# Performance work log

Measured on AMD Instinct MI355X. Metric: run time of the kernel, lower is better.

Reference implementation:

```python
import jax, jax.numpy as jnp
from jax import lax
import numpy as np

FACTOR = 2
KERNEL = 3  # conv kernel size (odd)
DN = ('NCDHW', 'OIDHW', 'NCDHW')


def _setup_fir_kernel():
    # resample_kernel = (1,3,3,1); separable outer product, normalized, * factor**3 gain
    k1 = jnp.asarray([1.0, 3.0, 3.0, 1.0], dtype=jnp.float32)
    k = jnp.einsum('i,j,k->ijk', k1, k1, k1)
    k = k / jnp.sum(k)
    return k * (FACTOR ** 3)  # [4,4,4]


def _upfirdn3d_1x1(x, k, pad0, pad1):
    # upfirdn3d with up=down=1: pad then depthwise-correlate with flipped FIR kernel
    # (torch code runs F.conv3d with torch.flip(kernel)).
    n, c = x.shape[0], x.shape[1]
    xp = jnp.pad(x, ((0, 0), (0, 0), (pad0, pad1), (pad0, pad1), (pad0, pad1)))
    kf = jnp.flip(k).astype(x.dtype)  # flip all 3 spatial axes
    w = jnp.broadcast_to(kf[None, None], (c, 1) + k.shape)  # depthwise [C,1,4,4,4]
    return lax.conv_general_dilated(xp, w, (1, 1, 1), 'VALID',
                                    dimension_numbers=DN,
                                    feature_group_count=c)


def _upsample_conv_3d(x, weight):
    # Equivalent of upsample_conv_3d(x, w, k=(1,3,3,1), factor=2):
    # torch flips the weight and feeds conv_transpose3d(stride=2); the flip and
    # the implicit transpose-flip cancel, so it equals an lhs-dilated correlation
    # with the ORIGINAL weight, padded by (k-1) on each side (output_padding=0).
    k = _setup_fir_kernel()
    p = k.shape[0] - FACTOR - (KERNEL - 1)  # = 0
    pad_lo, pad_hi = (p + 1) // 2 + FACTOR - 1, p // 2 + 1  # = (1, 1)
    y = lax.conv_general_dilated(
        x, weight.astype(x.dtype), (1, 1, 1),
        padding=[(KERNEL - 1, KERNEL - 1)] * 3,
        lhs_dilation=(FACTOR, FACTOR, FACTOR),
        dimension_numbers=DN)  # [N, outC, 33, 33, 33]
    return _upfirdn3d_1x1(y, k, pad_lo, pad_hi)  # [N, outC, 32, 32, 32]


def setup_inputs() -> dict:
    key = jax.random.key(0)
    k1, k2, k3 = jax.random.split(key, 3)
    x = jax.random.normal(k1, (8, 256, 16, 16, 16), dtype=jnp.float32)
    weight = jax.random.normal(k2, (128, 256, 3, 3, 3), dtype=jnp.float32) * 0.05
    bias = jax.random.normal(k3, (128,), dtype=jnp.float32) * 0.05
    return {"x": x, "weight": weight, "bias": bias}


def reference(x, weight, bias):
    y = _upsample_conv_3d(x, weight)
    return y + bias.reshape(1, -1, 1, 1, 1)
```

## Files before the change

kernel.cpp:

```cpp
#include <hip/hip_runtime.h>
#include <string.h>

typedef __attribute__((ext_vector_type(4))) float f32x4;
typedef __attribute__((ext_vector_type(8))) _Float16 f16x8;
typedef unsigned short u16;
typedef unsigned int   u32;

#define NBATCH 8
#define ICN 256
#define OCN 128
#define VOLP 36432
#define WRE 884736
#define XTE 8388608
#define ZBF 4096
#define S1POOL 33792

__host__ __device__ constexpr int cls_yoff2(int c){
  return (c==0)?0:(c==1)?5168:(c==2)?9792:(c==3)?14416:
         (c==4)?18768:(c==5)?23632:(c==6)?27984:32336;
}
__host__ __device__ constexpr int cls_nxyp(int c){
  return ((c&3)==0)?304:((c&3)==3)?256:272;
}

__device__ __forceinline__ u16 f2h(float v){
  _Float16 h = (_Float16)v;
  u16 u; memcpy(&u, &h, 2);
  return u;
}

#define GLOAD16(gp, lp)                                                        \
  __builtin_amdgcn_global_load_lds(                                            \
      (const __attribute__((address_space(1))) void*)(gp),                     \
      (__attribute__((address_space(3))) void*)(lp), 16, 0, 0)

__global__ __launch_bounds__(256) void prep_w(const float* __restrict__ w,
                                              u16* __restrict__ wh,
                                              float* __restrict__ zb){
  if (blockIdx.x < 16) zb[blockIdx.x*256 + threadIdx.x] = 0.f;
  int idx = blockIdx.x*256 + threadIdx.x;
  int e = idx&7, ln=(idx>>3)&63, og=(idx>>9)&7, icc=(idx>>12)&7, tt=idx>>15;
  int oc = og*16 + (ln&15);
  int ic = icc*32 + ((ln>>4)&3)*8 + e;
  const int toffs[8] = {0,8,12,16,18,22,24,26};
  const int tcnt[8]  = {8,4,4,2,4,2,2,1};
  int c=0, t=0;
  #pragma unroll
  for (int cc=0; cc<8; ++cc)
    if (tt>=toffs[cc] && tt<toffs[cc]+tcnt[cc]){ c=cc; t=tt-toffs[cc]; }
  int ez=c>>2, ey=(c>>1)&1, ex=c&1;
  int ty=2-ey, tx=2-ex;
  int ax=t%tx, ay=(t/tx)%ty, az=t/(tx*ty);
  int qz = ez?1:(az?2:0), qy = ey?1:(ay?2:0), qx = ex?1:(ax?2:0);
  wh[idx] = f2h(w[((size_t)oc*ICN + ic)*27 + (qz*3+qy)*3+qx]);
}

__global__ __launch_bounds__(256) void prep_x(const float* __restrict__ x,
                                              u16* __restrict__ xh){
  u32 o = blockIdx.x*256 + threadIdx.x;
  int il = o & 31, p = (o>>5)&4095, icc = (o>>17)&7, n = o>>20;
  xh[o] = f2h(x[(size_t)(n*256 + icc*32 + il)*4096 + p]);
}

#define S1_ISSUE(BUFBYTE, ICCV, AZV)                                           \
  {                                                                            \
    _Pragma("unroll")                                                          \
    for (int j_=0; j_<3; ++j_){                                                \
      const int r_ = j_*64 + ln;                                               \
      if (r_ < 170){                                                           \
        const int s_ = wv*170 + r_;                                            \
        const int icg_ = s_&3, pos_ = s_>>2;                                   \
        const int xi_ = pos_%17, yi_ = pos_/17;                                \
        const int zc_ = EZ ? mz : (mz-1+(AZV));                                \
        const int yc_ = my0 + yi_ + (EY-1);                                    \
        const int xc_ = xi_ + (EX-1);                                          \
        const bool inb_ = (u32)zc_<16u && (u32)yc_<16u && (u32)xc_<16u;        \
        const size_t g_ = nbase + (size_t)(ICCV)*131072                        \
                        + (size_t)((zc_*256+yc_*16+xc_)*32 + icg_*8);          \
        const u16* gh_ = inb_ ? (xh+g_) : zb16;                                \
        char* lh_ = pool + (BUFBYTE) + s_*16;                                  \
        GLOAD16(gh_, lh_);                                                     \
      }                                                                        \
    }                                                                          \
  }

template<int EZ,int EY,int EX>
__device__ __forceinline__ void s1body(char* pool,
                                       const u16* __restrict__ xh,
                                       const u16* __restrict__ wh,
                                       const u16* __restrict__ zb16,
                                       float* __restrict__ yd, int n0, int mt, int mz, int nl, int tid)
{
  constexpr int TZ=2-EZ, TY=2-EY, TX=2-EX;
  constexpr int DX=17-EX;
  constexpr int DY=17-EY;
  constexpr int NXY=DY*DX;
  constexpr int CLS = EZ*4+EY*2+EX;
  constexpr int YOFF = cls_yoff2(CLS);
  constexpr int NXYP = cls_nxyp(CLS);
  constexpr int W27 = (CLS==0)?0:(CLS==1)?8:(CLS==2)?12:(CLS==3)?16:
                      (CLS==4)?18:(CLS==5)?22:(CLS==6)?24:26;
  constexpr int NST = TZ*8;
  u16* AsU = (u16*)pool;

  const int wv=tid>>6, ln=tid&63;
  const int mhalf = wv&1, ochalf = wv>>1;
  const int my0=(mt*128)/DX;

  int posA[4];
  #pragma unroll
  for (int fi=0; fi<4; ++fi){
    int m = mt*128 + mhalf*64 + fi*16 + (ln&15);
    if (m > NXY-1) m = NXY-1;
    int my=m/DX, mx=m-my*DX;
    posA[fi] = ((my-my0)*17 + mx)*32 + (ln>>4)*8;
  }

  f32x4 acc[4][4];
  #pragma unroll
  for (int i=0;i<4;++i)
    #pragma unroll
    for (int j=0;j<4;++j) acc[i][j]=(f32x4){0.f,0.f,0.f,0.f};

  const size_t nbase = (size_t)(n0+nl)*(ICN*4096);

  S1_ISSUE(0, 0, 0);

  int st = 0;
  #pragma unroll 1
  for (int icc=0; icc<8; ++icc){
    #pragma unroll
    for (int az=0; az<TZ; ++az){
      const int cur = st & 1;
      const bool have_next = (st+1) < NST;
      if (have_next){
        const int nicc = (az+1<TZ)?icc:(icc+1);
        const int naz  = (az+1<TZ)?(az+1):0;
        S1_ISSUE((cur^1)*10880, nicc, naz);
        asm volatile("s_waitcnt vmcnt(3)" ::: "memory");
      } else {
        asm volatile("s_waitcnt vmcnt(0)" ::: "memory");
      }
      asm volatile("s_barrier" ::: "memory");
      const int curo = cur*5440;

      #pragma unroll
      for (int ay=0; ay<TY; ++ay)
      #pragma unroll
      for (int ax=0; ax<TX; ++ax){
        const int t = (az*TY+ay)*TX+ax;
        const int toff = (ay*17+ax)*32;
        f16x8 ah[4];
        #pragma unroll
        for (int fi=0; fi<4; ++fi)
          ah[fi] = *(const f16x8*)&AsU[curo + posA[fi]+toff];
        const u16* bp = wh + (size_t)(((W27+t)*8+icc)*8)*512 + (ochalf*4)*512 + ln*8;
        f16x8 bh[4];
        #pragma unroll
        for (int og=0; og<4; ++og) bh[og] = *(const f16x8*)(bp + og*512);
        #pragma unroll
        for (int fi=0; fi<4; ++fi)
          #pragma unroll
          for (int og=0; og<4; ++og)
            acc[fi][og] = __builtin_amdgcn_mfma_f32_16x16x32_f16(ah[fi], bh[og], acc[fi][og],0,0,0);
      }
      asm volatile("s_barrier" ::: "memory");
      ++st;
    }
  }

  float* tr = (float*)pool + wv*(64*33);
  #pragma unroll
  for (int pass=0; pass<2; ++pass){
    #pragma unroll
    for (int fi=0; fi<2; ++fi)
      #pragma unroll
      for (int og=0; og<4; ++og)
        #pragma unroll
        for (int j=0; j<4; ++j)
          tr[(og*16+(ln&15))*33 + fi*16 + (ln>>4)*4 + j] = acc[pass*2+fi][og][j];
    int m = mt*128 + mhalf*64 + pass*32 + (ln&31);
    bool valid = m < NXY;
    size_t lbase = (size_t)YOFF + (size_t)mz*NXYP + (valid ? m : 0);
    #pragma unroll 4
    for (int i=0; i<32; ++i){
      int r = 2*i + (ln>>5);
      float v = tr[r*33 + (ln&31)];
      int oc = ochalf*64 + r;
      if (valid)
        __builtin_nontemporal_store(v, yd + (size_t)(nl*128 + oc)*VOLP + lbase);
    }
  }
}

__global__ __launch_bounds__(256,3) void stage1f(const u16* __restrict__ xh,
                                                 const u16* __restrict__ wh,
                                                 const u16* __restrict__ zb16,
                                                 float* __restrict__ yd, int n0){
  __shared__ __align__(16) char pool[S1POOL];
  int bid = blockIdx.x, nl, tid = threadIdx.x;
  if (gridDim.z == 1){ nl = bid & 7; bid >>= 3; }
  else               { nl = blockIdx.z; }
  int mz, sub;
  if (bid < 352){ mz = bid/22; sub = bid - mz*22; }
  else          { mz = 16;     sub = bid - 352;   }
  if      (sub <  3) s1body<0,0,0>(pool,xh,wh,zb16,yd,n0,sub   ,mz,nl,tid);
  else if (sub <  6) s1body<0,0,1>(pool,xh,wh,zb16,yd,n0,sub- 3,mz,nl,tid);
  else if (sub <  9) s1body<0,1,0>(pool,xh,wh,zb16,yd,n0,sub- 6,mz,nl,tid);
  else if (sub < 11) s1body<0,1,1>(pool,xh,wh,zb16,yd,n0,sub- 9,mz,nl,tid);
  else if (sub < 14) s1body<1,0,0>(pool,xh,wh,zb16,yd,n0,sub-11,mz,nl,tid);
  else if (sub < 17) s1body<1,0,1>(pool,xh,wh,zb16,yd,n0,sub-14,mz,nl,tid);
  else if (sub < 20) s1body<1,1,0>(pool,xh,wh,zb16,yd,n0,sub-17,mz,nl,tid);
  else               s1body<1,1,1>(pool,xh,wh,zb16,yd,n0,sub-20,mz,nl,tid);
}

__global__ __launch_bounds__(256) void stage2d(const float* __restrict__ yd, const float* __restrict__ bias,
                                               float* __restrict__ out, int n0){
  __shared__ float raw[33][36];
  __shared__ float fx[35][36];
  const int tid=threadIdx.x;
  const int zg=blockIdx.x, oc=blockIdx.y, nl=blockIdx.z;
  const float* yb = yd + (size_t)(nl*128+oc)*VOLP;
  const float b = bias[oc];
  float* ob = out + (size_t)((n0+nl)*128+oc)*32768;
  for (int t2=tid; t2<1188; t2+=256) raw[t2/36][t2%36] = 0.f;
  if (tid < 72){ fx[(tid>=36)?34:0][tid%36] = 0.f; }
  __syncthreads();
  float a0[4]={0,0,0,0}, a1[4]={0,0,0,0}, a2[4]={0,0,0,0};
  #pragma unroll 1
  for (int s=0; s<19; ++s){
    int uz = zg*16 - 1 + s;
    if ((u32)uz < 33u){
      const int cz = uz & 1, zi = uz >> 1;
      #pragma unroll
      for (int cy=0; cy<2; ++cy)
        #pragma unroll
        for (int cx=0; cx<2; ++cx){
          const int DXc = 17-cx;
          const int NXYc = (17-cy)*DXc;
          const int NXYPc = cls_nxyp(cy*2+cx);
          const int yoff = (cz ? cls_yoff2(4+cy*2+cx) : cls_yoff2(cy*2+cx)) + zi*NXYPc;
          const float* sp = yb + yoff;
          for (int s2=tid; s2<NXYc; s2+=256){
            int r = s2/DXc, c2 = s2 - r*DXc;
            raw[2*r+cy][2*c2+cx+1] = __builtin_nontemporal_load(sp + s2);
          }
        }
    } else {
      for (int t2=tid; t2<1188; t2+=256) raw[t2/36][t2%36] = 0.f;
    }
    __syncthreads();
    for (int t2=tid; t2<1056; t2+=256){
      int uy = t2>>5, ox = t2&31;
      fx[uy+1][ox] = 0.25f*raw[uy][ox] + 0.75f*raw[uy][ox+1]
                   + 0.75f*raw[uy][ox+2] + 0.25f*raw[uy][ox+3];
    }
    __syncthreads();
    #pragma unroll
    for (int k=0;k<4;++k){
      int pos = tid + k*256;
      int oy = pos>>5, ox = pos&31;
      float fv = 0.25f*fx[oy][ox] + 0.75f*fx[oy+1][ox]
               + 0.75f*fx[oy+2][ox] + 0.25f*fx[oy+3][ox];
      if (s >= 3){
        int oz = zg*16 + s - 3;
        __builtin_nontemporal_store(a0[k] + 0.25f*fv + b, ob + (size_t)oz*1024 + pos);
      }
      a0[k] = a1[k] + 0.75f*fv;
      a1[k] = a2[k] + 0.75f*fv;
      a2[k] = 0.25f*fv;
    }
    __syncthreads();
  }
}

extern "C" void kernel_launch(void* const* d_in, const int* in_sizes, int n_in,
                              void* d_out, int out_size, void* d_ws, size_t ws_size,
                              hipStream_t stream) {
  const float* x    = (const float*)d_in[0];
  const float* w    = (const float*)d_in[1];
  const float* bias = (const float*)d_in[2];
  float* out = (float*)d_out;

  float* zb = (float*)d_ws;
  u16* wh = (u16*)(zb + ZBF);
  u16* xh = wh + WRE;
  float* yd = (float*)(xh + XTE);
  size_t base = (size_t)ZBF*4 + (size_t)(WRE + XTE)*2;

  int nChunk = 1;
  if      (ws_size >= base + (size_t)8*128*VOLP*4) nChunk=8;
  else if (ws_size >= base + (size_t)4*128*VOLP*4) nChunk=4;
  else if (ws_size >= base + (size_t)2*128*VOLP*4) nChunk=2;

  prep_w<<<dim3(WRE/256), 256, 0, stream>>>(w, wh, zb);
  prep_x<<<dim3(XTE/256), 256, 0, stream>>>(x, xh);

  const u16* zb16 = (const u16*)zb;
  if (nChunk == 8){
    stage1f<<<dim3(2904,1,1),256,0,stream>>>(xh,wh,zb16,yd,0);
    stage2d<<<dim3(2,128,8),256,0,stream>>>(yd,bias,out,0);
  } else {
    for (int n0=0; n0<NBATCH; n0+=nChunk){
      stage1f<<<dim3(363,1,nChunk),256,0,stream>>>(xh,wh,zb16,yd,n0);
      stage2d<<<dim3(2,128,nChunk),256,0,stream>>>(yd,bias,out,n0);
    }
  }
}
```

Measured before the change: 226.9 us.

## Enlarge stage1 M tiles, store intermediate in fp16, split stage2 finer

Stage1 blocks now cover 256 output positions (FI=8 fragments per wave, with small remainder variants), and each B-weight load is reused across twice as many MFMAs. The grid shrinks from 2904 to 1848 blocks and occupancy drops to 2 blocks per CU. The intermediate y buffer is now stored as fp16 instead of fp32, halving its write and read traffic at some precision cost. Stage2 splits z into 4 groups instead of 2 for more parallelism, and s_setprio is placed around the MFMA section.

```diff
diff --git a/kernel.cpp b/kernel.cpp
--- a/kernel.cpp
+++ b/kernel.cpp
@@ -13,7 +13,7 @@
 #define WRE 884736
 #define XTE 8388608
 #define ZBF 4096
-#define S1POOL 33792
+#define S1POOL 39168
 
 __host__ __device__ constexpr int cls_yoff2(int c){
   return (c==0)?0:(c==1)?5168:(c==2)?9792:(c==3)?14416:
@@ -28,11 +28,21 @@
   u16 u; memcpy(&u, &h, 2);
   return u;
 }
+__device__ __forceinline__ float h2f(u16 u){
+  _Float16 h; memcpy(&h, &u, 2);
+  return (float)h;
+}
 
 #define GLOAD16(gp, lp)                                                        \
   __builtin_amdgcn_global_load_lds(                                            \
       (const __attribute__((address_space(1))) void*)(gp),                     \
       (__attribute__((address_space(3))) void*)(lp), 16, 0, 0)
+
+template<int N> __device__ __forceinline__ void waitcnt_vm(){
+  if constexpr (N==0) asm volatile("s_waitcnt vmcnt(0)" ::: "memory");
+  else if constexpr (N==2) asm volatile("s_waitcnt vmcnt(2)" ::: "memory");
+  else if constexpr (N==5) asm volatile("s_waitcnt vmcnt(5)" ::: "memory");
+}
 
 __global__ __launch_bounds__(256) void prep_w(const float* __restrict__ w,
                                               u16* __restrict__ wh,
@@ -65,10 +75,10 @@
 #define S1_ISSUE(BUFBYTE, ICCV, AZV)                                           \
   {                                                                            \
     _Pragma("unroll")                                                          \
-    for (int j_=0; j_<3; ++j_){                                                \
+    for (int j_=0; j_<KITER; ++j_){                                            \
       const int r_ = j_*64 + ln;                                               \
-      if (r_ < 170){                                                           \
-        const int s_ = wv*170 + r_;                                            \
+      if (r_ < PERW){                                                          \
+        const int s_ = wv*PERW + r_;                                           \
         const int icg_ = s_&3, pos_ = s_>>2;                                   \
         const int xi_ = pos_%17, yi_ = pos_/17;                                \
         const int zc_ = EZ ? mz : (mz-1+(AZV));                                \
@@ -84,12 +94,12 @@
     }                                                                          \
   }
 
-template<int EZ,int EY,int EX>
+template<int EZ,int EY,int EX,int FI>
 __device__ __forceinline__ void s1body(char* pool,
                                        const u16* __restrict__ xh,
                                        const u16* __restrict__ wh,
                                        const u16* __restrict__ zb16,
-                                       float* __restrict__ yd, int n0, int mt, int mz, int nl, int tid)
+                                       u16* __restrict__ yd, int n0, int mt, int mz, int nl, int tid)
 {
   constexpr int TZ=2-EZ, TY=2-EY, TX=2-EX;
   constexpr int DX=17-EX;
@@ -100,25 +110,32 @@
   constexpr int NXYP = cls_nxyp(CLS);
   constexpr int W27 = (CLS==0)?0:(CLS==1)?8:(CLS==2)?12:(CLS==3)?16:
                       (CLS==4)?18:(CLS==5)?22:(CLS==6)?24:26;
-  constexpr int NST = TZ*8;
+  constexpr int ROWS  = (FI==8)?18:4;
+  constexpr int APOSP = ROWS*17;
+  constexpr int NCH   = APOSP*4;
+  constexpr int PERW  = NCH/4;
+  constexpr int KITER = (PERW+63)/64;
+  constexpr int BUFB  = NCH*16;
+  constexpr int NST   = TZ*8;
   u16* AsU = (u16*)pool;
 
   const int wv=tid>>6, ln=tid&63;
   const int mhalf = wv&1, ochalf = wv>>1;
-  const int my0=(mt*128)/DX;
-
-  int posA[4];
+  const int my0 = (mt*256)/DX;
+  const int mbase = mt*256 + ((FI==8)? mhalf*128 : 0);
+
+  int posA[FI];
   #pragma unroll
-  for (int fi=0; fi<4; ++fi){
-    int m = mt*128 + mhalf*64 + fi*16 + (ln&15);
+  for (int fi=0; fi<FI; ++fi){
+    int m = mbase + fi*16 + (ln&15);
     if (m > NXY-1) m = NXY-1;
     int my=m/DX, mx=m-my*DX;
     posA[fi] = ((my-my0)*17 + mx)*32 + (ln>>4)*8;
   }
 
-  f32x4 acc[4][4];
+  f32x4 acc[FI][4];
   #pragma unroll
-  for (int i=0;i<4;++i)
+  for (int i=0;i<FI;++i)
     #pragma unroll
     for (int j=0;j<4;++j) acc[i][j]=(f32x4){0.f,0.f,0.f,0.f};
 
@@ -136,56 +153,61 @@
       if (have_next){
         const int nicc = (az+1<TZ)?icc:(icc+1);
         const int naz  = (az+1<TZ)?(az+1):0;
-        S1_ISSUE((cur^1)*10880, nicc, naz);
-        asm volatile("s_waitcnt vmcnt(3)" ::: "memory");
+        S1_ISSUE((cur^1)*BUFB, nicc, naz);
+        waitcnt_vm<KITER>();
       } else {
-        asm volatile("s_waitcnt vmcnt(0)" ::: "memory");
+        waitcnt_vm<0>();
       }
       asm volatile("s_barrier" ::: "memory");
-      const int curo = cur*5440;
-
+      const int curo = cur*(BUFB/2);
+
+      __builtin_amdgcn_s_setprio(1);
       #pragma unroll
       for (int ay=0; ay<TY; ++ay)
       #pragma unroll
       for (int ax=0; ax<TX; ++ax){
         const int t = (az*TY+ay)*TX+ax;
         const int toff = (ay*17+ax)*32;
-        f16x8 ah[4];
-        #pragma unroll
-        for (int fi=0; fi<4; ++fi)
-          ah[fi] = *(const f16x8*)&AsU[curo + posA[fi]+toff];
         const u16* bp = wh + (size_t)(((W27+t)*8+icc)*8)*512 + (ochalf*4)*512 + ln*8;
         f16x8 bh[4];
         #pragma unroll
         for (int og=0; og<4; ++og) bh[og] = *(const f16x8*)(bp + og*512);
         #pragma unroll
-        for (int fi=0; fi<4; ++fi)
+        for (int fi=0; fi<FI; ++fi){
+          f16x8 ah = *(const f16x8*)&AsU[curo + posA[fi]+toff];
           #pragma unroll
           for (int og=0; og<4; ++og)
-            acc[fi][og] = __builtin_amdgcn_mfma_f32_16x16x32_f16(ah[fi], bh[og], acc[fi][og],0,0,0);
+            acc[fi][og] = __builtin_amdgcn_mfma_f32_16x16x32_f16(ah, bh[og], acc[fi][og],0,0,0);
+        }
       }
+      __builtin_amdgcn_s_setprio(0);
       asm volatile("s_barrier" ::: "memory");
       ++st;
     }
   }
 
   float* tr = (float*)pool + wv*(64*33);
+  constexpr int NPASS = (FI+1)/2;
   #pragma unroll
-  for (int pass=0; pass<2; ++pass){
+  for (int pass=0; pass<NPASS; ++pass){
     #pragma unroll
-    for (int fi=0; fi<2; ++fi)
-      #pragma unroll
-      for (int og=0; og<4; ++og)
+    for (int fi2=0; fi2<2; ++fi2){
+      if (pass*2+fi2 < FI){
         #pragma unroll
-        for (int j=0; j<4; ++j)
-          tr[(og*16+(ln&15))*33 + fi*16 + (ln>>4)*4 + j] = acc[pass*2+fi][og][j];
-    int m = mt*128 + mhalf*64 + pass*32 + (ln&31);
-    bool valid = m < NXY;
+        for (int og=0; og<4; ++og)
+          #pragma unroll
+          for (int j=0; j<4; ++j)
+            tr[(og*16+(ln&15))*33 + fi2*16 + (ln>>4)*4 + j] = acc[pass*2+fi2][og][j];
+      }
+    }
+    const int mcol = pass*32 + (ln&31);
+    const int m = mbase + mcol;
+    const bool valid = (m < NXY) && (mcol < FI*16) && (FI==8 || mhalf==0);
     size_t lbase = (size_t)YOFF + (size_t)mz*NXYP + (valid ? m : 0);
     #pragma unroll 4
     for (int i=0; i<32; ++i){
       int r = 2*i + (ln>>5);
-      float v = tr[r*33 + (ln&31)];
+      u16 v = f2h(tr[r*33 + (ln&31)]);
       int oc = ochalf*64 + r;
       if (valid)
         __builtin_nontemporal_store(v, yd + (size_t)(nl*128 + oc)*VOLP + lbase);
@@ -193,34 +215,47 @@
   }
 }
 
-__global__ __launch_bounds__(256,3) void stage1f(const u16* __restrict__ xh,
+__global__ __launch_bounds__(256,2) void stage1f(const u16* __restrict__ xh,
                                                  const u16* __restrict__ wh,
                                                  const u16* __restrict__ zb16,
-                                                 float* __restrict__ yd, int n0){
+                                                 u16* __restrict__ yd, int n0){
   __shared__ __align__(16) char pool[S1POOL];
   int bid = blockIdx.x, nl, tid = threadIdx.x;
   if (gridDim.z == 1){ nl = bid & 7; bid >>= 3; }
   else               { nl = blockIdx.z; }
-  int mz, sub;
-  if (bid < 352){ mz = bid/22; sub = bid - mz*22; }
-  else          { mz = 16;     sub = bid - 352;   }
-  if      (sub <  3) s1body<0,0,0>(pool,xh,wh,zb16,yd,n0,sub   ,mz,nl,tid);
-  else if (sub <  6) s1body<0,0,1>(pool,xh,wh,zb16,yd,n0,sub- 3,mz,nl,tid);
-  else if (sub <  9) s1body<0,1,0>(pool,xh,wh,zb16,yd,n0,sub- 6,mz,nl,tid);
-  else if (sub < 11) s1body<0,1,1>(pool,xh,wh,zb16,yd,n0,sub- 9,mz,nl,tid);
-  else if (sub < 14) s1body<1,0,0>(pool,xh,wh,zb16,yd,n0,sub-11,mz,nl,tid);
-  else if (sub < 17) s1body<1,0,1>(pool,xh,wh,zb16,yd,n0,sub-14,mz,nl,tid);
-  else if (sub < 20) s1body<1,1,0>(pool,xh,wh,zb16,yd,n0,sub-17,mz,nl,tid);
-  else               s1body<1,1,1>(pool,xh,wh,zb16,yd,n0,sub-20,mz,nl,tid);
-}
-
-__global__ __launch_bounds__(256) void stage2d(const float* __restrict__ yd, const float* __restrict__ bias,
+  int mz, sub, ez;
+  if (bid < 119){ ez = 0; mz = bid/7;  sub = bid - mz*7; }
+  else          { int b2 = bid-119; ez = 1; mz = b2/7; sub = b2 - mz*7; }
+  if (ez == 0){
+    switch(sub){
+      case 0: s1body<0,0,0,8>(pool,xh,wh,zb16,yd,n0,0,mz,nl,tid); break;
+      case 1: s1body<0,0,0,3>(pool,xh,wh,zb16,yd,n0,1,mz,nl,tid); break;
+      case 2: s1body<0,0,1,8>(pool,xh,wh,zb16,yd,n0,0,mz,nl,tid); break;
+      case 3: s1body<0,0,1,1>(pool,xh,wh,zb16,yd,n0,1,mz,nl,tid); break;
+      case 4: s1body<0,1,0,8>(pool,xh,wh,zb16,yd,n0,0,mz,nl,tid); break;
+      case 5: s1body<0,1,0,1>(pool,xh,wh,zb16,yd,n0,1,mz,nl,tid); break;
+      default:s1body<0,1,1,8>(pool,xh,wh,zb16,yd,n0,0,mz,nl,tid); break;
+    }
+  } else {
+    switch(sub){
+      case 0: s1body<1,0,0,8>(pool,xh,wh,zb16,yd,n0,0,mz,nl,tid); break;
+      case 1: s1body<1,0,0,3>(pool,xh,wh,zb16,yd,n0,1,mz,nl,tid); break;
+      case 2: s1body<1,0,1,8>(pool,xh,wh,zb16,yd,n0,0,mz,nl,tid); break;
+      case 3: s1body<1,0,1,1>(pool,xh,wh,zb16,yd,n0,1,mz,nl,tid); break;
+      case 4: s1body<1,1,0,8>(pool,xh,wh,zb16,yd,n0,0,mz,nl,tid); break;
+      case 5: s1body<1,1,0,1>(pool,xh,wh,zb16,yd,n0,1,mz,nl,tid); break;
+      default:s1body<1,1,1,8>(pool,xh,wh,zb16,yd,n0,0,mz,nl,tid); break;
+    }
+  }
+}
+
+__global__ __launch_bounds__(256) void stage2d(const u16* __restrict__ yd, const float* __restrict__ bias,
                                                float* __restrict__ out, int n0){
   __shared__ float raw[33][36];
   __shared__ float fx[35][36];
   const int tid=threadIdx.x;
   const int zg=blockIdx.x, oc=blockIdx.y, nl=blockIdx.z;
-  const float* yb = yd + (size_t)(nl*128+oc)*VOLP;
+  const u16* yb = yd + (size_t)(nl*128+oc)*VOLP;
   const float b = bias[oc];
   float* ob = out + (size_t)((n0+nl)*128+oc)*32768;
   for (int t2=tid; t2<1188; t2+=256) raw[t2/36][t2%36] = 0.f;
@@ -228,8 +263,8 @@
   __syncthreads();
   float a0[4]={0,0,0,0}, a1[4]={0,0,0,0}, a2[4]={0,0,0,0};
   #pragma unroll 1
-  for (int s=0; s<19; ++s){
-    int uz = zg*16 - 1 + s;
+  for (int s=0; s<11; ++s){
+    int uz = zg*8 - 1 + s;
     if ((u32)uz < 33u){
       const int cz = uz & 1, zi = uz >> 1;
       #pragma unroll
@@ -240,10 +275,10 @@
           const int NXYc = (17-cy)*DXc;
           const int NXYPc = cls_nxyp(cy*2+cx);
           const int yoff = (cz ? cls_yoff2(4+cy*2+cx) : cls_yoff2(cy*2+cx)) + zi*NXYPc;
-          const float* sp = yb + yoff;
+          const u16* sp = yb + yoff;
           for (int s2=tid; s2<NXYc; s2+=256){
             int r = s2/DXc, c2 = s2 - r*DXc;
-            raw[2*r+cy][2*c2+cx+1] = __builtin_nontemporal_load(sp + s2);
+            raw[2*r+cy][2*c2+cx+1] = h2f(__builtin_nontemporal_load(sp + s2));
           }
         }
     } else {
@@ -263,7 +298,7 @@
       float fv = 0.25f*fx[oy][ox] + 0.75f*fx[oy+1][ox]
                + 0.75f*fx[oy+2][ox] + 0.25f*fx[oy+3][ox];
       if (s >= 3){
-        int oz = zg*16 + s - 3;
+        int oz = zg*8 + s - 3;
         __builtin_nontemporal_store(a0[k] + 0.25f*fv + b, ob + (size_t)oz*1024 + pos);
       }
       a0[k] = a1[k] + 0.75f*fv;
@@ -285,25 +320,25 @@
   float* zb = (float*)d_ws;
   u16* wh = (u16*)(zb + ZBF);
   u16* xh = wh + WRE;
-  float* yd = (float*)(xh + XTE);
+  u16* yd = xh + XTE;
   size_t base = (size_t)ZBF*4 + (size_t)(WRE + XTE)*2;
 
   int nChunk = 1;
-  if      (ws_size >= base + (size_t)8*128*VOLP*4) nChunk=8;
-  else if (ws_size >= base + (size_t)4*128*VOLP*4) nChunk=4;
-  else if (ws_size >= base + (size_t)2*128*VOLP*4) nChunk=2;
+  if      (ws_size >= base + (size_t)8*128*VOLP*2) nChunk=8;
+  else if (ws_size >= base + (size_t)4*128*VOLP*2) nChunk=4;
+  else if (ws_size >= base + (size_t)2*128*VOLP*2) nChunk=2;
 
   prep_w<<<dim3(WRE/256), 256, 0, stream>>>(w, wh, zb);
   prep_x<<<dim3(XTE/256), 256, 0, stream>>>(x, xh);
 
   const u16* zb16 = (const u16*)zb;
   if (nChunk == 8){
-    stage1f<<<dim3(2904,1,1),256,0,stream>>>(xh,wh,zb16,yd,0);
-    stage2d<<<dim3(2,128,8),256,0,stream>>>(yd,bias,out,0);
+    stage1f<<<dim3(1848,1,1),256,0,stream>>>(xh,wh,zb16,yd,0);
+    stage2d<<<dim3(4,128,8),256,0,stream>>>(yd,bias,out,0);
   } else {
     for (int n0=0; n0<NBATCH; n0+=nChunk){
-      stage1f<<<dim3(363,1,nChunk),256,0,stream>>>(xh,wh,zb16,yd,n0);
-      stage2d<<<dim3(2,128,nChunk),256,0,stream>>>(yd,bias,out,n0);
-    }
-  }
-}
+      stage1f<<<dim3(231,1,nChunk),256,0,stream>>>(xh,wh,zb16,yd,n0);
+      stage2d<<<dim3(4,128,nChunk),256,0,stream>>>(yd,bias,out,n0);
+    }
+  }
+}
```

After: 255.5 us. 1.13x slower.

## Store intermediate conv output in fp16 and split FIR stage per output z-pair

Applied to the files above, without the earlier changes.

The stage-1 intermediate buffer is now written as fp16 instead of fp32, which halves the bytes written by stage1 and read by stage2. Stage2 is also restructured: each block now computes one pair of output z-slices from 5 input slices instead of streaming 19 slices through a rolling accumulator. That gives an 8x larger grid for more parallelism. The cost is about 2.5x redundant reads of the intermediate across z and an extra rounding step to fp16 that may reduce accuracy.

```diff
diff --git a/kernel.cpp b/kernel.cpp
--- a/kernel.cpp
+++ b/kernel.cpp
@@ -27,6 +27,10 @@
   _Float16 h = (_Float16)v;
   u16 u; memcpy(&u, &h, 2);
   return u;
+}
+__device__ __forceinline__ float h2f(u16 u){
+  _Float16 h; memcpy(&h, &u, 2);
+  return (float)h;
 }
 
 #define GLOAD16(gp, lp)                                                        \
@@ -89,7 +93,7 @@
                                        const u16* __restrict__ xh,
                                        const u16* __restrict__ wh,
                                        const u16* __restrict__ zb16,
-                                       float* __restrict__ yd, int n0, int mt, int mz, int nl, int tid)
+                                       u16* __restrict__ yd, int n0, int mt, int mz, int nl, int tid)
 {
   constexpr int TZ=2-EZ, TY=2-EY, TX=2-EX;
   constexpr int DX=17-EX;
@@ -185,7 +189,7 @@
     #pragma unroll 4
     for (int i=0; i<32; ++i){
       int r = 2*i + (ln>>5);
-      float v = tr[r*33 + (ln&31)];
+      u16 v = f2h(tr[r*33 + (ln&31)]);
       int oc = ochalf*64 + r;
       if (valid)
         __builtin_nontemporal_store(v, yd + (size_t)(nl*128 + oc)*VOLP + lbase);
@@ -196,7 +200,7 @@
 __global__ __launch_bounds__(256,3) void stage1f(const u16* __restrict__ xh,
                                                  const u16* __restrict__ wh,
                                                  const u16* __restrict__ zb16,
-                                                 float* __restrict__ yd, int n0){
+                                                 u16* __restrict__ yd, int n0){
   __shared__ __align__(16) char pool[S1POOL];
   int bid = blockIdx.x, nl, tid = threadIdx.x;
   if (gridDim.z == 1){ nl = bid & 7; bid >>= 3; }
@@ -214,24 +218,26 @@
   else               s1body<1,1,1>(pool,xh,wh,zb16,yd,n0,sub-20,mz,nl,tid);
 }
 
-__global__ __launch_bounds__(256) void stage2d(const float* __restrict__ yd, const float* __restrict__ bias,
+__global__ __launch_bounds__(256) void stage2d(const u16* __restrict__ yd, const float* __restrict__ bias,
                                                float* __restrict__ out, int n0){
   __shared__ float raw[33][36];
   __shared__ float fx[35][36];
   const int tid=threadIdx.x;
-  const int zg=blockIdx.x, oc=blockIdx.y, nl=blockIdx.z;
-  const float* yb = yd + (size_t)(nl*128+oc)*VOLP;
+  const int zi=blockIdx.x, oc=blockIdx.y, nl=blockIdx.z;
+  const u16* yb = yd + (size_t)(nl*128+oc)*VOLP;
   const float b = bias[oc];
   float* ob = out + (size_t)((n0+nl)*128+oc)*32768;
   for (int t2=tid; t2<1188; t2+=256) raw[t2/36][t2%36] = 0.f;
   if (tid < 72){ fx[(tid>=36)?34:0][tid%36] = 0.f; }
   __syncthreads();
-  float a0[4]={0,0,0,0}, a1[4]={0,0,0,0}, a2[4]={0,0,0,0};
-  #pragma unroll 1
-  for (int s=0; s<19; ++s){
-    int uz = zg*16 - 1 + s;
+  float acc0[4]={0,0,0,0}, acc1[4]={0,0,0,0};
+  #pragma unroll
+  for (int p=0; p<5; ++p){
+    const float K0 = (p==0||p==3)?0.25f:(p==1||p==2)?0.75f:0.f;
+    const float K1 = (p==1||p==4)?0.25f:(p==2||p==3)?0.75f:0.f;
+    int uz = 2*zi - 1 + p;
     if ((u32)uz < 33u){
-      const int cz = uz & 1, zi = uz >> 1;
+      const int cz = uz & 1, zi2 = uz >> 1;
       #pragma unroll
       for (int cy=0; cy<2; ++cy)
         #pragma unroll
@@ -239,11 +245,11 @@
           const int DXc = 17-cx;
           const int NXYc = (17-cy)*DXc;
           const int NXYPc = cls_nxyp(cy*2+cx);
-          const int yoff = (cz ? cls_yoff2(4+cy*2+cx) : cls_yoff2(cy*2+cx)) + zi*NXYPc;
-          const float* sp = yb + yoff;
+          const int yoff = (cz ? cls_yoff2(4+cy*2+cx) : cls_yoff2(cy*2+cx)) + zi2*NXYPc;
+          const u16* sp = yb + yoff;
           for (int s2=tid; s2<NXYc; s2+=256){
             int r = s2/DXc, c2 = s2 - r*DXc;
-            raw[2*r+cy][2*c2+cx+1] = __builtin_nontemporal_load(sp + s2);
+            raw[2*r+cy][2*c2+cx+1] = h2f(__builtin_nontemporal_load(sp + s2));
           }
         }
     } else {
@@ -262,15 +268,16 @@
       int oy = pos>>5, ox = pos&31;
       float fv = 0.25f*fx[oy][ox] + 0.75f*fx[oy+1][ox]
                + 0.75f*fx[oy+2][ox] + 0.25f*fx[oy+3][ox];
-      if (s >= 3){
-        int oz = zg*16 + s - 3;
-        __builtin_nontemporal_store(a0[k] + 0.25f*fv + b, ob + (size_t)oz*1024 + pos);
-      }
-      a0[k] = a1[k] + 0.75f*fv;
-      a1[k] = a2[k] + 0.75f*fv;
-      a2[k] = 0.25f*fv;
+      acc0[k] += K0*fv;
+      acc1[k] += K1*fv;
     }
     __syncthreads();
+  }
+  #pragma unroll
+  for (int k=0;k<4;++k){
+    int pos = tid + k*256;
+    __builtin_nontemporal_store(acc0[k] + b, ob + (size_t)(2*zi  )*1024 + pos);
+    __builtin_nontemporal_store(acc1[k] + b, ob + (size_t)(2*zi+1)*1024 + pos);
   }
 }
 
@@ -285,13 +292,13 @@
   float* zb = (float*)d_ws;
   u16* wh = (u16*)(zb + ZBF);
   u16* xh = wh + WRE;
-  float* yd = (float*)(xh + XTE);
+  u16* yd = xh + XTE;
   size_t base = (size_t)ZBF*4 + (size_t)(WRE + XTE)*2;
 
   int nChunk = 1;
-  if      (ws_size >= base + (size_t)8*128*VOLP*4) nChunk=8;
-  else if (ws_size >= base + (size_t)4*128*VOLP*4) nChunk=4;
-  else if (ws_size >= base + (size_t)2*128*VOLP*4) nChunk=2;
+  if      (ws_size >= base + (size_t)8*128*VOLP*2) nChunk=8;
+  else if (ws_size >= base + (size_t)4*128*VOLP*2) nChunk=4;
+  else if (ws_size >= base + (size_t)2*128*VOLP*2) nChunk=2;
 
   prep_w<<<dim3(WRE/256), 256, 0, stream>>>(w, wh, zb);
   prep_x<<<dim3(XTE/256), 256, 0, stream>>>(x, xh);
@@ -299,11 +306,11 @@
   const u16* zb16 = (const u16*)zb;
   if (nChunk == 8){
     stage1f<<<dim3(2904,1,1),256,0,stream>>>(xh,wh,zb16,yd,0);
-    stage2d<<<dim3(2,128,8),256,0,stream>>>(yd,bias,out,0);
+    stage2d<<<dim3(16,128,8),256,0,stream>>>(yd,bias,out,0);
   } else {
     for (int n0=0; n0<NBATCH; n0+=nChunk){
       stage1f<<<dim3(363,1,nChunk),256,0,stream>>>(xh,wh,zb16,yd,n0);
-      stage2d<<<dim3(2,128,nChunk),256,0,stream>>>(yd,bias,out,n0);
-    }
-  }
-}
+      stage2d<<<dim3(16,128,nChunk),256,0,stream>>>(yd,bias,out,n0);
+    }
+  }
+}
```

Measured after the change: 384.3 us. 1.69x slower.
